# Optimization experiments

Measured on AMD Instinct MI355X. Metric: run time of the kernel, lower is better.

The kernel has to match this reference:

```python
import jax, jax.numpy as jnp
import numpy as np

B, C, H, W = 8, 256, 64, 64
OUT, K = 256, 3
OG = 1
STRIDE, PAD, DIL = 1, 1, 1
K2 = K * K


def setup_inputs() -> dict:
    key = jax.random.key(0)
    ks = jax.random.split(key, 5)
    x = jax.random.normal(ks[0], (B, C, H, W), jnp.float32)
    # main deform-conv weight [out, in//groups, k, k]
    weight = jax.random.normal(ks[1], (OUT, C, K, K), jnp.float32) * (1.0 / np.sqrt(C * K2))
    bias = jax.random.normal(ks[2], (OUT,), jnp.float32) * 0.01
    # param_generator: 3x3 conv -> 3*OG*K*K channels (oh, ow, mask)
    pg_w = jax.random.normal(ks[3], (3 * OG * K2, C, 3, 3), jnp.float32) * 0.01
    pg_b = jax.random.normal(ks[4], (3 * OG * K2,), jnp.float32) * 0.01
    return {"x": x, "weight": weight, "bias": bias, "pg_w": pg_w, "pg_b": pg_b}


def _conv3x3(x, w, b):
    y = jax.lax.conv_general_dilated(
        x, w, (1, 1), [(1, 1), (1, 1)],
        dimension_numbers=("NCHW", "OIHW", "NCHW"))
    return y + b[None, :, None, None]


def _bilinear_gather(img, py, px):
    # img [B,C,H,W]; py,px [B,K2,Ho,Wo] -> [B,C,K2,Ho,Wo]
    # Zero padding outside the image (torchvision deform_conv2d semantics).
    Hh, Ww = img.shape[2], img.shape[3]
    y0 = jnp.floor(py)
    x0 = jnp.floor(px)
    dy = py - y0
    dx = px - x0
    imgf = img.reshape(img.shape[0], img.shape[1], Hh * Ww)
    out = jnp.zeros((img.shape[0], img.shape[1]) + py.shape[1:], img.dtype)
    corners = (
        (0, 0, (1 - dy) * (1 - dx)),
        (0, 1, (1 - dy) * dx),
        (1, 0, dy * (1 - dx)),
        (1, 1, dy * dx),
    )
    for oy, ox, wgt in corners:
        yy = y0 + oy
        xx = x0 + ox
        valid = (yy >= 0) & (yy < Hh) & (xx >= 0) & (xx < Ww)
        yi = jnp.clip(yy, 0, Hh - 1).astype(jnp.int32)
        xi = jnp.clip(xx, 0, Ww - 1).astype(jnp.int32)
        idx = yi * Ww + xi  # [B,K2,Ho,Wo]
        g = jax.vmap(lambda im, ix: jnp.take(im, ix.reshape(-1), axis=1))(imgf, idx)
        g = g.reshape(img.shape[0], img.shape[1], *idx.shape[1:])
        out = out + g * (wgt * valid)[:, None]
    return out


def _deform_conv2d(x, weight, bias, pg_w, pg_b):
    Bn = x.shape[0]
    Hi, Wi = x.shape[2], x.shape[3]
    Ho = (Hi + 2 * PAD - DIL * (K - 1) - 1) // STRIDE + 1
    Wo = (Wi + 2 * PAD - DIL * (K - 1) - 1) // STRIDE + 1
    params = _conv3x3(x, pg_w, pg_b)  # [B, 3*OG*K2, H, W]
    oh, ow, mask = jnp.split(params, 3, axis=1)
    offset = jnp.concatenate([oh, ow], axis=1)  # [B, 2*OG*K2, Ho, Wo]
    mask = jax.nn.sigmoid(mask)                  # [B, OG*K2, Ho, Wo]
    # torchvision layout: channel = ((og*K2 + k)*2 + {y,x})
    off = offset.reshape(Bn, OG, K2, 2, Ho, Wo)
    dy = off[:, :, :, 0].reshape(Bn, K2, Ho, Wo)  # OG == 1
    dx = off[:, :, :, 1].reshape(Bn, K2, Ho, Wo)
    hy = jnp.arange(Ho, dtype=x.dtype) * STRIDE - PAD
    wx = jnp.arange(Wo, dtype=x.dtype) * STRIDE - PAD
    ky, kx = jnp.meshgrid(jnp.arange(K), jnp.arange(K), indexing="ij")
    base_y = hy[None, :, None] + (ky.reshape(-1) * DIL).astype(x.dtype)[:, None, None]  # [K2,Ho,1]
    base_x = wx[None, None, :] + (kx.reshape(-1) * DIL).astype(x.dtype)[:, None, None]  # [K2,1,Wo]
    py = dy + base_y[None]  # [B,K2,Ho,Wo]
    px = dx + base_x[None]
    sampled = _bilinear_gather(x, py, px)          # [B,C,K2,Ho,Wo]
    sampled = sampled * mask[:, None]              # modulation (OG=1)
    out = jnp.einsum("bckhw,ock->bohw", sampled, weight.reshape(OUT, C, K2))
    return out + bias[None, :, None, None]


def reference(x, weight, bias, pg_w, pg_b):
    return _deform_conv2d(x, weight, bias, pg_w, pg_b)
```

## Files before the change

### kernel.cpp

```cpp
#include <hip/hip_runtime.h>
#include <math.h>

#define BQ   8
#define CIN  256
#define HH   64
#define WW   64
#define COUT 256
#define K2   9
#define PCH  27

#define PT     64
#define CCH    32
#define NCHUNK (CIN / CCH)
#define NSTEP  72
#define NSUB   24
#define SUBROW 104
#define PLANE  (HH * WW)

typedef __attribute__((ext_vector_type(8))) short short8;
typedef __attribute__((ext_vector_type(4))) float f32x4;
typedef __attribute__((ext_vector_type(2))) float f32x2;

#define PIPE_BARRIER() do {                                   \
    asm volatile("s_waitcnt lgkmcnt(0)" ::: "memory");        \
    __builtin_amdgcn_s_barrier();                             \
    asm volatile("" ::: "memory");                            \
} while (0)

static __device__ __forceinline__ unsigned short f2bf(float f) {
    unsigned u = __builtin_bit_cast(unsigned, f);
    u += 0x7fff + ((u >> 16) & 1);
    return (unsigned short)(u >> 16);
}
static __device__ __forceinline__ f32x2 up2(unsigned u) {
    f32x2 r;
    r[0] = __builtin_bit_cast(float, u << 16);
    r[1] = __builtin_bit_cast(float, u & 0xffff0000u);
    return r;
}
static __device__ __forceinline__ unsigned cvtpk(float lo, float hi) {
    unsigned r;
    asm("v_cvt_pk_bf16_f32 %0, %1, %2" : "=v"(r) : "v"(lo), "v"(hi));
    return r;
}

__global__ __launch_bounds__(256) void k_packw(const float* __restrict__ w,
                                               unsigned short* __restrict__ wp) {
    int t = blockIdx.x * 256 + threadIdx.x;
    if (t >= NSTEP * COUT * 4) return;
    int q = t & 3;
    int o = (t >> 2) & 255;
    int s = t >> 10;
    short8 sv;
#pragma unroll
    for (int j = 0; j < 8; ++j) {
        int pos   = s * 32 + q * 8 + j;
        int chunk = pos / (CCH * K2);
        int pl    = pos % (CCH * K2);
        int ktap  = pl >> 5;
        int c     = chunk * CCH + (pl & 31);
        sv[j] = (short)f2bf(w[(o * CIN + c) * K2 + ktap]);
    }
    *(short8*)(wp + (size_t)t * 8) = sv;
}

__global__ __launch_bounds__(256) void k_packpg(const float* __restrict__ pgw,
                                                unsigned short* __restrict__ wpg) {
    int t = blockIdx.x * 256 + threadIdx.x;
    if (t >= NSTEP * 32 * 4) return;
    int q = t & 3;
    int o = (t >> 2) & 31;
    int s = t >> 7;
    short8 sv;
#pragma unroll
    for (int j = 0; j < 8; ++j) {
        int pos   = s * 32 + q * 8 + j;
        int chunk = pos / (CCH * K2);
        int pl    = pos % (CCH * K2);
        int ktap  = pl >> 5;
        int c     = chunk * CCH + (pl & 31);
        sv[j] = (o < PCH) ? (short)f2bf(pgw[(size_t)(o * CIN + c) * K2 + ktap]) : (short)0;
    }
    *(short8*)(wpg + (size_t)t * 8) = sv;
}

__global__ __launch_bounds__(256) void k_xt(const float* __restrict__ x,
                                            unsigned short* __restrict__ xT) {
    __shared__ float tile[64][65];
    int blk = blockIdx.x;
    int cc  = blk & 3;
    int y   = (blk >> 2) & 63;
    int b   = blk >> 8;
    int t   = threadIdx.x;
    int c0  = cc * 64;

    const float* xp = x + ((size_t)(b * CIN + c0) * HH + y) * WW;
#pragma unroll
    for (int r = 0; r < 16; ++r) {
        int cl = r * 4 + (t >> 6);
        int xx = t & 63;
        tile[cl][xx] = xp[(size_t)cl * PLANE + xx];
    }
    __syncthreads();
    unsigned short* op = xT + ((size_t)b * PLANE + (size_t)y * WW) * CIN + c0;
#pragma unroll
    for (int r = 0; r < 16; ++r) {
        int xx = r * 4 + (t >> 6);
        int cl = t & 63;
        op[(size_t)xx * CIN + cl] = f2bf(tile[cl][xx]);
    }
}

__global__ __launch_bounds__(512, 4) void k_params(const unsigned short* __restrict__ xT,
                                                   const unsigned short* __restrict__ wpg,
                                                   const float* __restrict__ pgb,
                                                   float* __restrict__ pv) {
    __shared__ alignas(16) unsigned short s_rows[3][66][40];

    int blk = blockIdx.x;
    int swz = (blk & 7) * 64 + (blk >> 3);
    int b   = swz >> 6;
    int h   = swz & 63;
    int t   = threadIdx.x;

    int wv  = t >> 6;
    int lm  = t & 15;
    int lq  = (t >> 4) & 3;
    int ipg = wv >> 2;
    int rpg = wv & 3;

    const unsigned short* xTb = xT + (size_t)b * PLANE * CIN;

    if (t < 24) {
        int ky  = t >> 3;
        int rem = t & 7;
        int col = (rem >> 2) * 65;
        int q   = rem & 3;
        uint4 z = make_uint4(0, 0, 0, 0);
        *(uint4*)&s_rows[ky][col][q * 8] = z;
    }
    __syncthreads();

    f32x4 accA = (f32x4){0.f, 0.f, 0.f, 0.f};
    f32x4 accB = (f32x4){0.f, 0.f, 0.f, 0.f};

    int pxm1 = t >> 3;
    int cgs  = (t & 7) * 4;

    for (int ch = 0; ch < NCHUNK; ++ch) {
#pragma unroll
        for (int ky = 0; ky < 3; ++ky) {
            int y = h + ky - 1;
            uint2 d = make_uint2(0, 0);
            if ((unsigned)y < (unsigned)HH)
                d = *(const uint2*)(xTb + (size_t)(y * WW + pxm1) * CIN + ch * CCH + cgs);
            *(uint2*)&s_rows[ky][pxm1 + 1][cgs] = d;
        }
        __syncthreads();
#pragma unroll
        for (int tap = 0; tap < K2; ++tap) {
            int ky = tap / 3, kx = tap % 3;
            short8 a  = *(const short8*)(wpg + (size_t)(ch * K2 + tap) * 32 * 32
                                         + (ipg * 16 + lm) * 32 + lq * 8);
            short8 bf = *(const short8*)&s_rows[ky][rpg * 16 + lm + kx][lq * 8];
            if (tap & 1)
                accB = __builtin_amdgcn_mfma_f32_16x16x32_bf16(a, bf, accB, 0, 0, 0);
            else
                accA = __builtin_amdgcn_mfma_f32_16x16x32_bf16(a, bf, accA, 0, 0, 0);
        }
        __syncthreads();
    }

    f32x4 accpg = accA + accB;
    int px = rpg * 16 + lm;
#pragma unroll
    for (int rg = 0; rg < 4; ++rg) {
        int oc = ipg * 16 + lq * 4 + rg;
        if (oc < PCH)
            pv[((size_t)(b * PCH + oc) << 12) + h * WW + px] = accpg[rg] + pgb[oc];
    }
}

__global__ __launch_bounds__(512, 4) void k_fused(const unsigned short* __restrict__ xT,
                                                  const unsigned short* __restrict__ wp,
                                                  const float* __restrict__ pv,
                                                  const float* __restrict__ bias,
                                                  float* __restrict__ out) {
    __shared__ alignas(16) unsigned short s_samp[2][PT][SUBROW];
    __shared__ float4 s_wgt4[K2][PT];
    __shared__ int4   s_off4[K2][PT];

    int blk = blockIdx.x;
    int swz = (blk & 7) * 64 + (blk >> 3);
    int b   = swz >> 6;
    int h   = swz & 63;
    int t   = threadIdx.x;

    int gp = t >> 3;
    int cg = t & 7;
    int wv = t >> 6;
    int lm = t & 15;
    int lq = (t >> 4) & 3;

    const char* xTb = (const char*)xT + (size_t)b * PLANE * CIN * 2;

    const float* pvb = pv + ((size_t)(b * PCH) << 12) + h * WW;
    for (int e = t; e < K2 * PT; e += 512) {
        int k = e >> 6;
        int p = e & 63;
        float dy = pvb[(size_t)(2 * k) << 12 | (unsigned)p];
        float dx = pvb[(size_t)(2 * k + 1) << 12 | (unsigned)p];
        float mz = pvb[(size_t)(18 + k) << 12 | (unsigned)p];
        float m  = 1.f / (1.f + expf(-mz));

        float py = dy + (float)(h - 1 + k / 3);
        float px = dx + (float)(p - 1 + k % 3);
        float y0f = floorf(py), x0f = floorf(px);
        float fy = py - y0f,    fx = px - x0f;
        int iy0 = (int)y0f, ix0 = (int)x0f;
        int iy1 = iy0 + 1,  ix1 = ix0 + 1;
        bool vy0 = (unsigned)iy0 < (unsigned)HH;
        bool vy1 = (unsigned)iy1 < (unsigned)HH;
        bool vx0 = (unsigned)ix0 < (unsigned)WW;
        bool vx1 = (unsigned)ix1 < (unsigned)WW;

        float w00 = (1.f - fy) * (1.f - fx) * m; if (!(vy0 && vx0)) w00 = 0.f;
        float w01 = (1.f - fy) * fx         * m; if (!(vy0 && vx1)) w01 = 0.f;
        float w10 = fy         * (1.f - fx) * m; if (!(vy1 && vx0)) w10 = 0.f;
        float w11 = fy         * fx         * m; if (!(vy1 && vx1)) w11 = 0.f;

        int cy0 = min(max(iy0, 0), HH - 1), cy1 = min(max(iy1, 0), HH - 1);
        int cx0 = min(max(ix0, 0), WW - 1), cx1 = min(max(ix1, 0), WW - 1);

        s_wgt4[k][p] = make_float4(w00, w01, w10, w11);
        s_off4[k][p] = make_int4((cy0 * WW + cx0) * 512, (cy0 * WW + cx1) * 512,
                                 (cy1 * WW + cx0) * 512, (cy1 * WW + cx1) * 512);
    }
    __syncthreads();

    int ow = wv * 32;
    f32x4 acc[2][4];
#pragma unroll
    for (int i = 0; i < 2; ++i)
#pragma unroll
        for (int j = 0; j < 4; ++j) acc[i][j] = (f32x4){0.f, 0.f, 0.f, 0.f};

    uint2 G[3][4];
    {
#pragma unroll
        for (int j = 0; j < 3; ++j) {
            int4 ob = s_off4[j][gp];
            G[j][0] = *(const uint2*)(xTb + ob.x + cg * 8);
            G[j][1] = *(const uint2*)(xTb + ob.y + cg * 8);
            G[j][2] = *(const uint2*)(xTb + ob.z + cg * 8);
            G[j][3] = *(const uint2*)(xTb + ob.w + cg * 8);
        }
#pragma unroll
        for (int j = 0; j < 3; ++j) {
            float4 gw = s_wgt4[j][gp];
            f32x2 v01 = gw.x * up2(G[j][0].x) + gw.y * up2(G[j][1].x)
                      + gw.z * up2(G[j][2].x) + gw.w * up2(G[j][3].x);
            f32x2 v23 = gw.x * up2(G[j][0].y) + gw.y * up2(G[j][1].y)
                      + gw.z * up2(G[j][2].y) + gw.w * up2(G[j][3].y);
            uint2 pk;
            pk.x = cvtpk(v01[0], v01[1]);
            pk.y = cvtpk(v23[0], v23[1]);
            *(uint2*)&s_samp[0][gp][j * 32 + cg * 4] = pk;
        }
#pragma unroll
        for (int j = 0; j < 3; ++j) {
            int4 ob = s_off4[3 + j][gp];
            G[j][0] = *(const uint2*)(xTb + ob.x + cg * 8);
            G[j][1] = *(const uint2*)(xTb + ob.y + cg * 8);
            G[j][2] = *(const uint2*)(xTb + ob.z + cg * 8);
            G[j][3] = *(const uint2*)(xTb + ob.w + cg * 8);
        }
        PIPE_BARRIER();
    }

    short8 a0c = *(const short8*)(wp + (ow +  0 + lm) * 32 + lq * 8);
    short8 a1c = *(const short8*)(wp + (ow + 16 + lm) * 32 + lq * 8);
    for (int sc = 0; sc < NSUB; ++sc) {
        bool doC = (sc + 1 < NSUB);
        bool doL = (sc + 2 < NSUB);
        int t1 = ((sc + 1) % 3) * 3;
        int t2 = ((sc + 2) % 3) * 3;
        int c2 = ((sc + 2) / 3) * (CCH * 2) + cg * 8;
        unsigned short (*__restrict__ bc)[SUBROW] = s_samp[sc & 1];
        unsigned short (*__restrict__ bn)[SUBROW] = s_samp[(sc + 1) & 1];
#pragma unroll
        for (int sl = 0; sl < 3; ++sl) {
            short8 b0 = *(const short8*)&bc[ 0 + lm][sl * 32 + lq * 8];
            short8 b1 = *(const short8*)&bc[16 + lm][sl * 32 + lq * 8];
            short8 b2 = *(const short8*)&bc[32 + lm][sl * 32 + lq * 8];
            short8 b3 = *(const short8*)&bc[48 + lm][sl * 32 + lq * 8];
            int r = sc * 3 + sl + 1;
            short8 a0n = a0c, a1n = a1c;
            if (r < NSTEP) {
                const unsigned short* wrn = wp + (size_t)r * COUT * 32;
                a0n = *(const short8*)(wrn + (ow +  0 + lm) * 32 + lq * 8);
                a1n = *(const short8*)(wrn + (ow + 16 + lm) * 32 + lq * 8);
            }
            if (doC) {
                float4 gw = s_wgt4[t1 + sl][gp];
                f32x2 v01 = gw.x * up2(G[sl][0].x) + gw.y * up2(G[sl][1].x)
                          + gw.z * up2(G[sl][2].x) + gw.w * up2(G[sl][3].x);
                f32x2 v23 = gw.x * up2(G[sl][0].y) + gw.y * up2(G[sl][1].y)
                          + gw.z * up2(G[sl][2].y) + gw.w * up2(G[sl][3].y);
                uint2 pk;
                pk.x = cvtpk(v01[0], v01[1]);
                pk.y = cvtpk(v23[0], v23[1]);
                *(uint2*)&bn[gp][sl * 32 + cg * 4] = pk;
            }
            if (doL) {
                int4 ob = s_off4[t2 + sl][gp];
                G[sl][0] = *(const uint2*)(xTb + ob.x + c2);
                G[sl][1] = *(const uint2*)(xTb + ob.y + c2);
                G[sl][2] = *(const uint2*)(xTb + ob.z + c2);
                G[sl][3] = *(const uint2*)(xTb + ob.w + c2);
            }
            __builtin_amdgcn_s_setprio(1);
            acc[0][0] = __builtin_amdgcn_mfma_f32_16x16x32_bf16(a0c, b0, acc[0][0], 0, 0, 0);
            acc[0][1] = __builtin_amdgcn_mfma_f32_16x16x32_bf16(a0c, b1, acc[0][1], 0, 0, 0);
            acc[0][2] = __builtin_amdgcn_mfma_f32_16x16x32_bf16(a0c, b2, acc[0][2], 0, 0, 0);
            acc[0][3] = __builtin_amdgcn_mfma_f32_16x16x32_bf16(a0c, b3, acc[0][3], 0, 0, 0);
            acc[1][0] = __builtin_amdgcn_mfma_f32_16x16x32_bf16(a1c, b0, acc[1][0], 0, 0, 0);
            acc[1][1] = __builtin_amdgcn_mfma_f32_16x16x32_bf16(a1c, b1, acc[1][1], 0, 0, 0);
            acc[1][2] = __builtin_amdgcn_mfma_f32_16x16x32_bf16(a1c, b2, acc[1][2], 0, 0, 0);
            acc[1][3] = __builtin_amdgcn_mfma_f32_16x16x32_bf16(a1c, b3, acc[1][3], 0, 0, 0);
            __builtin_amdgcn_s_setprio(0);
            a0c = a0n; a1c = a1n;
        }
        PIPE_BARRIER();
    }

    float* op = out + ((size_t)b * COUT) * PLANE + h * WW;
#pragma unroll
    for (int i = 0; i < 2; ++i) {
        int o0 = ow + i * 16 + lq * 4;
        f32x4 bv = *(const f32x4*)(bias + o0);
#pragma unroll
        for (int rg = 0; rg < 4; ++rg) {
#pragma unroll
            for (int j = 0; j < 4; ++j)
                op[(size_t)(o0 + rg) * PLANE + j * 16 + lm] = acc[i][j][rg] + bv[rg];
        }
    }
}

extern "C" void kernel_launch(void* const* d_in, const int* in_sizes, int n_in,
                              void* d_out, int out_size, void* d_ws, size_t ws_size,
                              hipStream_t stream) {
    const float* x    = (const float*)d_in[0];
    const float* wgt  = (const float*)d_in[1];
    const float* bias = (const float*)d_in[2];
    const float* pgw  = (const float*)d_in[3];
    const float* pgb  = (const float*)d_in[4];
    float* out = (float*)d_out;

    const size_t WPK_B = (size_t)NSTEP * COUT * 32 * 2;
    const size_t WPG_B = (size_t)NSTEP * 32 * 32 * 2;
    const size_t XT_B  = (size_t)BQ * PLANE * CIN * 2;
    unsigned short* wpk = (unsigned short*)d_ws;
    unsigned short* wpg = (unsigned short*)((char*)d_ws + WPK_B);
    unsigned short* xT  = (unsigned short*)((char*)d_ws + WPK_B + WPG_B);
    float*          pv  = (float*)((char*)d_ws + WPK_B + WPG_B + XT_B);

    k_packw <<<(NSTEP * COUT * 4 + 255) / 256, 256, 0, stream>>>(wgt, wpk);
    k_packpg<<<(NSTEP * 32 * 4 + 255) / 256,   256, 0, stream>>>(pgw, wpg);
    k_xt    <<<BQ * HH * 4, 256, 0, stream>>>(x, xT);
    k_params<<<BQ * HH, 512, 0, stream>>>(xT, wpg, pgb, pv);
    k_fused <<<BQ * HH, 512, 0, stream>>>(xT, wpk, pv, bias, out);
}
```

Measured before the change: 118.7 us.

## Merge prep kernels and double-buffer k_params LDS with register prefetch

Merges the three preprocessing kernels (x transpose, weight pack, param-weight pack) into one launch that dispatches on block index, cutting two launches and their gaps. In k_params, the LDS row buffer becomes double-buffered and the next channel chunk is prefetched into registers while the current one is consumed, so the trailing barrier per chunk goes away. The launch-bounds occupancy hint for k_params drops from 4 to 2 blocks per CU, and LDS use doubles.

```diff
diff --git a/kernel.cpp b/kernel.cpp
--- a/kernel.cpp
+++ b/kernel.cpp
@@ -17,6 +17,11 @@
 #define SUBROW 104
 #define PLANE  (HH * WW)
 
+#define NXT    (BQ * HH * 4)
+#define NPW    ((NSTEP * COUT * 4) / 256)
+#define NPG    ((NSTEP * 32 * 4) / 256)
+#define NPREP  (NXT + NPW + NPG)
+
 typedef __attribute__((ext_vector_type(8))) short short8;
 typedef __attribute__((ext_vector_type(4))) float f32x4;
 typedef __attribute__((ext_vector_type(2))) float f32x2;
@@ -44,78 +49,77 @@
     return r;
 }
 
-__global__ __launch_bounds__(256) void k_packw(const float* __restrict__ w,
-                                               unsigned short* __restrict__ wp) {
-    int t = blockIdx.x * 256 + threadIdx.x;
-    if (t >= NSTEP * COUT * 4) return;
-    int q = t & 3;
-    int o = (t >> 2) & 255;
-    int s = t >> 10;
-    short8 sv;
-#pragma unroll
-    for (int j = 0; j < 8; ++j) {
-        int pos   = s * 32 + q * 8 + j;
-        int chunk = pos / (CCH * K2);
-        int pl    = pos % (CCH * K2);
-        int ktap  = pl >> 5;
-        int c     = chunk * CCH + (pl & 31);
-        sv[j] = (short)f2bf(w[(o * CIN + c) * K2 + ktap]);
-    }
-    *(short8*)(wp + (size_t)t * 8) = sv;
-}
-
-__global__ __launch_bounds__(256) void k_packpg(const float* __restrict__ pgw,
-                                                unsigned short* __restrict__ wpg) {
-    int t = blockIdx.x * 256 + threadIdx.x;
-    if (t >= NSTEP * 32 * 4) return;
-    int q = t & 3;
-    int o = (t >> 2) & 31;
-    int s = t >> 7;
-    short8 sv;
-#pragma unroll
-    for (int j = 0; j < 8; ++j) {
-        int pos   = s * 32 + q * 8 + j;
-        int chunk = pos / (CCH * K2);
-        int pl    = pos % (CCH * K2);
-        int ktap  = pl >> 5;
-        int c     = chunk * CCH + (pl & 31);
-        sv[j] = (o < PCH) ? (short)f2bf(pgw[(size_t)(o * CIN + c) * K2 + ktap]) : (short)0;
-    }
-    *(short8*)(wpg + (size_t)t * 8) = sv;
-}
-
-__global__ __launch_bounds__(256) void k_xt(const float* __restrict__ x,
-                                            unsigned short* __restrict__ xT) {
+__global__ __launch_bounds__(256) void k_prep(const float* __restrict__ x,
+                                              unsigned short* __restrict__ xT,
+                                              const float* __restrict__ w,
+                                              unsigned short* __restrict__ wp,
+                                              const float* __restrict__ pgw,
+                                              unsigned short* __restrict__ wpg) {
     __shared__ float tile[64][65];
     int blk = blockIdx.x;
-    int cc  = blk & 3;
-    int y   = (blk >> 2) & 63;
-    int b   = blk >> 8;
-    int t   = threadIdx.x;
-    int c0  = cc * 64;
-
-    const float* xp = x + ((size_t)(b * CIN + c0) * HH + y) * WW;
-#pragma unroll
-    for (int r = 0; r < 16; ++r) {
-        int cl = r * 4 + (t >> 6);
-        int xx = t & 63;
-        tile[cl][xx] = xp[(size_t)cl * PLANE + xx];
-    }
-    __syncthreads();
-    unsigned short* op = xT + ((size_t)b * PLANE + (size_t)y * WW) * CIN + c0;
-#pragma unroll
-    for (int r = 0; r < 16; ++r) {
-        int xx = r * 4 + (t >> 6);
-        int cl = t & 63;
-        op[(size_t)xx * CIN + cl] = f2bf(tile[cl][xx]);
-    }
-}
-
-__global__ __launch_bounds__(512, 4) void k_params(const unsigned short* __restrict__ xT,
+
+    if (blk < NXT) {
+        int cc  = blk & 3;
+        int y   = (blk >> 2) & 63;
+        int b   = blk >> 8;
+        int t   = threadIdx.x;
+        int c0  = cc * 64;
+
+        const float* xp = x + ((size_t)(b * CIN + c0) * HH + y) * WW;
+#pragma unroll
+        for (int r = 0; r < 16; ++r) {
+            int cl = r * 4 + (t >> 6);
+            int xx = t & 63;
+            tile[cl][xx] = xp[(size_t)cl * PLANE + xx];
+        }
+        __syncthreads();
+        unsigned short* op = xT + ((size_t)b * PLANE + (size_t)y * WW) * CIN + c0;
+#pragma unroll
+        for (int r = 0; r < 16; ++r) {
+            int xx = r * 4 + (t >> 6);
+            int cl = t & 63;
+            op[(size_t)xx * CIN + cl] = f2bf(tile[cl][xx]);
+        }
+    } else if (blk < NXT + NPW) {
+        int t = (blk - NXT) * 256 + threadIdx.x;
+        int q = t & 3;
+        int o = (t >> 2) & 255;
+        int s = t >> 10;
+        short8 sv;
+#pragma unroll
+        for (int j = 0; j < 8; ++j) {
+            int pos   = s * 32 + q * 8 + j;
+            int chunk = pos / (CCH * K2);
+            int pl    = pos % (CCH * K2);
+            int ktap  = pl >> 5;
+            int c     = chunk * CCH + (pl & 31);
+            sv[j] = (short)f2bf(w[(o * CIN + c) * K2 + ktap]);
+        }
+        *(short8*)(wp + (size_t)t * 8) = sv;
+    } else {
+        int t = (blk - NXT - NPW) * 256 + threadIdx.x;
+        int q = t & 3;
+        int o = (t >> 2) & 31;
+        int s = t >> 7;
+        short8 sv;
+#pragma unroll
+        for (int j = 0; j < 8; ++j) {
+            int pos   = s * 32 + q * 8 + j;
+            int chunk = pos / (CCH * K2);
+            int pl    = pos % (CCH * K2);
+            int ktap  = pl >> 5;
+            int c     = chunk * CCH + (pl & 31);
+            sv[j] = (o < PCH) ? (short)f2bf(pgw[(size_t)(o * CIN + c) * K2 + ktap]) : (short)0;
+        }
+        *(short8*)(wpg + (size_t)t * 8) = sv;
+    }
+}
+
+__global__ __launch_bounds__(512, 2) void k_params(const unsigned short* __restrict__ xT,
                                                    const unsigned short* __restrict__ wpg,
                                                    const float* __restrict__ pgb,
                                                    float* __restrict__ pv) {
-    __shared__ alignas(16) unsigned short s_rows[3][66][40];
+    __shared__ alignas(16) unsigned short s_rows[2][3][66][40];
 
     int blk = blockIdx.x;
     int swz = (blk & 7) * 64 + (blk >> 3);
@@ -131,13 +135,15 @@
 
     const unsigned short* xTb = xT + (size_t)b * PLANE * CIN;
 
-    if (t < 24) {
-        int ky  = t >> 3;
-        int rem = t & 7;
+    if (t < 48) {
+        int bufk = t >= 24;
+        int tt  = t - bufk * 24;
+        int ky  = tt >> 3;
+        int rem = tt & 7;
         int col = (rem >> 2) * 65;
         int q   = rem & 3;
         uint4 z = make_uint4(0, 0, 0, 0);
-        *(uint4*)&s_rows[ky][col][q * 8] = z;
+        *(uint4*)&s_rows[bufk][ky][col][q * 8] = z;
     }
     __syncthreads();
 
@@ -147,14 +153,28 @@
     int pxm1 = t >> 3;
     int cgs  = (t & 7) * 4;
 
+    uint2 R[3];
+#pragma unroll
+    for (int ky = 0; ky < 3; ++ky) {
+        int y = h + ky - 1;
+        R[ky] = make_uint2(0, 0);
+        if ((unsigned)y < (unsigned)HH)
+            R[ky] = *(const uint2*)(xTb + (size_t)(y * WW + pxm1) * CIN + cgs);
+    }
+
     for (int ch = 0; ch < NCHUNK; ++ch) {
 #pragma unroll
-        for (int ky = 0; ky < 3; ++ky) {
-            int y = h + ky - 1;
-            uint2 d = make_uint2(0, 0);
-            if ((unsigned)y < (unsigned)HH)
-                d = *(const uint2*)(xTb + (size_t)(y * WW + pxm1) * CIN + ch * CCH + cgs);
-            *(uint2*)&s_rows[ky][pxm1 + 1][cgs] = d;
+        for (int ky = 0; ky < 3; ++ky)
+            *(uint2*)&s_rows[ch & 1][ky][pxm1 + 1][cgs] = R[ky];
+        if (ch + 1 < NCHUNK) {
+#pragma unroll
+            for (int ky = 0; ky < 3; ++ky) {
+                int y = h + ky - 1;
+                R[ky] = make_uint2(0, 0);
+                if ((unsigned)y < (unsigned)HH)
+                    R[ky] = *(const uint2*)(xTb + (size_t)(y * WW + pxm1) * CIN
+                                            + (ch + 1) * CCH + cgs);
+            }
         }
         __syncthreads();
 #pragma unroll
@@ -162,13 +182,12 @@
             int ky = tap / 3, kx = tap % 3;
             short8 a  = *(const short8*)(wpg + (size_t)(ch * K2 + tap) * 32 * 32
                                          + (ipg * 16 + lm) * 32 + lq * 8);
-            short8 bf = *(const short8*)&s_rows[ky][rpg * 16 + lm + kx][lq * 8];
+            short8 bf = *(const short8*)&s_rows[ch & 1][ky][rpg * 16 + lm + kx][lq * 8];
             if (tap & 1)
                 accB = __builtin_amdgcn_mfma_f32_16x16x32_bf16(a, bf, accB, 0, 0, 0);
             else
                 accA = __builtin_amdgcn_mfma_f32_16x16x32_bf16(a, bf, accA, 0, 0, 0);
         }
-        __syncthreads();
     }
 
     f32x4 accpg = accA + accB;
@@ -366,9 +385,7 @@
     unsigned short* xT  = (unsigned short*)((char*)d_ws + WPK_B + WPG_B);
     float*          pv  = (float*)((char*)d_ws + WPK_B + WPG_B + XT_B);
 
-    k_packw <<<(NSTEP * COUT * 4 + 255) / 256, 256, 0, stream>>>(wgt, wpk);
-    k_packpg<<<(NSTEP * 32 * 4 + 255) / 256,   256, 0, stream>>>(pgw, wpg);
-    k_xt    <<<BQ * HH * 4, 256, 0, stream>>>(x, xT);
+    k_prep  <<<NPREP, 256, 0, stream>>>(x, xT, wgt, wpk, pgw, wpg);
     k_params<<<BQ * HH, 512, 0, stream>>>(xT, wpg, pgb, pv);
     k_fused <<<BQ * HH, 512, 0, stream>>>(xT, wpk, pv, bias, out);
 }
```

Result: faster. 111.0 us (-6.5%).
